# Kernel optimization log

Hardware: AMD Instinct MI355X
Metric: run time of the kernel (lower is better)

## Reference

```python
import jax, jax.numpy as jnp
import numpy as np
from jax import lax

B, C, H, W = 2, 96, 48, 48
BASE_C, HEADS, D_STATE, D_CONV, EXPAND = 32, 8, 16, 4, 2
D_INNER = EXPAND * C          # 192 (mamba expand=2)
DT_RANK = (C + 15) // 16      # 6  (ceil(d_model/16))
LN_EPS = 1e-5


def setup_inputs() -> dict:
    key = jax.random.key(0)
    ks = jax.random.split(key, 16)
    g = lambda i, shape, s=0.02: jax.random.normal(ks[i], shape, jnp.float32) * s
    return {
        "x": jax.random.normal(ks[0], (B, C, H, W), jnp.float32),
        "f_lu": jax.random.normal(ks[1], (B, BASE_C, 12, 12), jnp.float32),
        "norm_w": jnp.ones((C,), jnp.float32),
        "norm_b": jnp.zeros((C,), jnp.float32),
        "qproj_w": g(2, (C, BASE_C)), "qproj_b": jnp.zeros((C,), jnp.float32),
        "iq_w": g(3, (C, C)), "iq_b": jnp.zeros((C,), jnp.float32),
        "ik_w": g(4, (C, C)), "ik_b": jnp.zeros((C,), jnp.float32),
        "iv_w": g(5, (C, C)), "iv_b": jnp.zeros((C,), jnp.float32),
        "io_w": g(6, (C, C)), "io_b": jnp.zeros((C,), jnp.float32),
        "m_in_w": g(7, (2 * D_INNER, C)),
        "m_conv_w": g(8, (D_INNER, 1, D_CONV), 0.1),
        "m_conv_b": jnp.zeros((D_INNER,), jnp.float32),
        "m_xproj_w": g(9, (DT_RANK + 2 * D_STATE, D_INNER)),
        "m_dtproj_w": g(10, (D_INNER, DT_RANK), 0.1),
        "m_dtproj_b": jnp.full((D_INNER,), -4.6, jnp.float32),  # softplus ~= 0.01
        "m_Alog": jnp.log(jnp.broadcast_to(
            jnp.arange(1, D_STATE + 1, dtype=jnp.float32), (D_INNER, D_STATE))),
        "m_D": jnp.ones((D_INNER,), jnp.float32),
        "m_out_w": g(11, (C, D_INNER)),
        "out_w": g(12, (C, C)), "out_b": jnp.zeros((C,), jnp.float32),
    }


def _pw(t, w, b):  # 1x1 conv
    return jnp.einsum('bchw,oc->bohw', t, w) + b[:, None, None]


def reference(x, f_lu, norm_w, norm_b, qproj_w, qproj_b,
              iq_w, iq_b, ik_w, ik_b, iv_w, iv_b, io_w, io_b,
              m_in_w, m_conv_w, m_conv_b, m_xproj_w, m_dtproj_w, m_dtproj_b,
              m_Alog, m_D, m_out_w, out_w, out_b):
    b, c, h, w = x.shape
    l = h * w
    dk = c // HEADS
    res = x

    # LayerNorm over channel dim
    xt = x.transpose(0, 2, 3, 1)
    mu = xt.mean(-1, keepdims=True)
    var = ((xt - mu) ** 2).mean(-1, keepdims=True)
    xn = ((xt - mu) * lax.rsqrt(var + LN_EPS) * norm_w + norm_b).transpose(0, 3, 1, 2)

    # bilinear upsample (align_corners=False) + 1x1 proj
    f = jax.image.resize(f_lu, (b, BASE_C, h, w), method='bilinear')
    f = _pw(f, qproj_w, qproj_b)

    # IAI cross-attention: query from f, key/value from normalized x
    q = _pw(f, iq_w, iq_b).reshape(b, HEADS, dk, l)
    k = _pw(xn, ik_w, ik_b).reshape(b, HEADS, dk, l)
    v = _pw(xn, iv_w, iv_b).reshape(b, HEADS, dk, l)
    attn = jax.nn.softmax(jnp.einsum('bhdl,bhdm->bhlm', q, k) * (dk ** -0.5), axis=-1)
    o = jnp.einsum('bhlm,bhdm->bhdl', attn, v).reshape(b, c, h, w)
    o = _pw(o, io_w, io_b)

    # ---- Mamba block (canonical mamba_ssm forward) ----
    def mamba(u):  # u: [Bm, L, C]
        Bm, L, _ = u.shape
        xz = jnp.einsum('blc,dc->bld', u, m_in_w)           # [Bm,L,2*D_INNER]
        xi, zg = xz[..., :D_INNER], xz[..., D_INNER:]
        # causal depthwise conv1d (d_conv=4) + SiLU
        xc = xi.transpose(0, 2, 1)                           # [Bm,D_INNER,L]
        xc = jnp.pad(xc, ((0, 0), (0, 0), (D_CONV - 1, 0)))
        xc = lax.conv_general_dilated(
            xc, m_conv_w, (1,), 'VALID',
            dimension_numbers=('NCH', 'OIH', 'NCH'),
            feature_group_count=D_INNER)
        xc = jax.nn.silu(xc + m_conv_b[None, :, None]).transpose(0, 2, 1)  # [Bm,L,D_INNER]
        x_dbl = jnp.einsum('bld,ed->ble', xc, m_xproj_w)
        dt = x_dbl[..., :DT_RANK]
        Bs = x_dbl[..., DT_RANK:DT_RANK + D_STATE]           # [Bm,L,N]
        Cs = x_dbl[..., DT_RANK + D_STATE:]                  # [Bm,L,N]
        dt = jax.nn.softplus(jnp.einsum('blr,dr->bld', dt, m_dtproj_w) + m_dtproj_b)
        A = -jnp.exp(m_Alog)                                 # [D_INNER,N]
        dA = jnp.exp(dt[..., None] * A)                      # [Bm,L,D_INNER,N]
        dBx = dt[..., None] * Bs[:, :, None, :] * xc[..., None]
        def comb(e1, e2):
            a1, b1 = e1
            a2, b2 = e2
            return a1 * a2, a2 * b1 + b2
        _, hs = lax.associative_scan(comb, (dA, dBx), axis=1)  # [Bm,L,D_INNER,N]
        y = jnp.einsum('bldn,bln->bld', hs, Cs) + m_D * xc
        y = y * jax.nn.silu(zg)
        return jnp.einsum('bld,cd->blc', y, m_out_w)

    # DSFS: four directional scans, averaged
    dirs = jnp.stack([o, jnp.flip(o, 3), jnp.flip(o, 2), jnp.flip(o, (2, 3))], 0)
    z = dirs.reshape(4 * b, c, l).transpose(0, 2, 1)         # [4b,l,c]
    y = mamba(z)
    y = y.transpose(0, 2, 1).reshape(4, b, c, h, w)
    y = (y[0] + jnp.flip(y[1], 3) + jnp.flip(y[2], 2) + jnp.flip(y[3], (2, 3))) / 4.0

    return _pw(y, out_w, out_b) + res
```

## Files before the change

### kernel.cpp

```cpp
#include <hip/hip_runtime.h>

static constexpr int B_ = 2, C_ = 96, H_ = 48, W_ = 48, L_ = 2304;
static constexpr int HEADS_ = 8, DK_ = 12, BASEC_ = 32;
static constexpr int DI_ = 192, DS_ = 16, DCONV_ = 4, DTR_ = 6;
static constexpr int NCH_ = 16, CHL_ = 144;
static constexpr int KC_ = 288;
static constexpr int KT2_ = 48;

__device__ __forceinline__ float sigmoidf_(float x){ return 1.f/(1.f+__expf(-x)); }

__global__ __launch_bounds__(256) void ln_kernel(const float* __restrict__ x,
    const float* __restrict__ nw, const float* __restrict__ nb, float* __restrict__ xn)
{
  __shared__ float tile[96][65];
  __shared__ float muS[64], rsS[64];
  int p0 = blockIdx.x * 64;
  int b  = p0 / L_;
  int hw0 = p0 % L_;
  int tid = threadIdx.x;
  for (int idx = tid; idx < 96*64; idx += 256) {
    int c = idx >> 6, i = idx & 63;
    tile[c][i] = x[((size_t)b*96 + c)*L_ + hw0 + i];
  }
  __syncthreads();
  if (tid < 64) {
    float s = 0.f;
    #pragma unroll 8
    for (int c = 0; c < 96; ++c) s += tile[c][tid];
    float mu = s * (1.f/96.f);
    float v = 0.f;
    #pragma unroll 8
    for (int c = 0; c < 96; ++c) { float d = tile[c][tid]-mu; v += d*d; }
    v *= (1.f/96.f);
    muS[tid] = mu;
    rsS[tid] = rsqrtf(v + 1e-5f);
  }
  __syncthreads();
  for (int idx = tid; idx < 96*64; idx += 256) {
    int i = idx / 96, c = idx % 96;
    float val = (tile[c][i]-muS[i])*rsS[i]*nw[c] + nb[c];
    xn[((size_t)(p0 + i))*96 + c] = val;
  }
}

__global__ __launch_bounds__(256) void resize_kernel(const float* __restrict__ f, float* __restrict__ o)
{
  int t = blockIdx.x*256 + threadIdx.x;
  if (t >= B_*L_*BASEC_) return;
  int c = t & 31;
  int p = t >> 5;
  int w = p % 48, h = (p/48) % 48, b = p / (48*48);
  const float* a = f + ((size_t)b*32 + c)*144;
  float sh = (h+0.5f)*0.25f - 0.5f;
  float sw = (w+0.5f)*0.25f - 0.5f;
  int h0 = (int)floorf(sh); float fh = sh - (float)h0;
  int w0 = (int)floorf(sw); float fw = sw - (float)w0;
  int h0c = min(max(h0,0),11), h1c = min(max(h0+1,0),11);
  int w0c = min(max(w0,0),11), w1c = min(max(w0+1,0),11);
  float v00 = a[h0c*12+w0c], v01 = a[h0c*12+w1c];
  float v10 = a[h1c*12+w0c], v11 = a[h1c*12+w1c];
  o[t] = (1.f-fh)*((1.f-fw)*v00 + fw*v01) + fh*((1.f-fw)*v10 + fw*v11);
}

__global__ __launch_bounds__(256) void gemm_k(
    const float* __restrict__ A, int lda,
    const float* __restrict__ W,
    const float* __restrict__ bias,
    float* __restrict__ Co,
    int M, int N, int K,
    int act, int smode,
    const float* __restrict__ resid)
{
  __shared__ __align__(16) float As[16][68];
  __shared__ __align__(16) float Ws[16][68];
  int m0 = blockIdx.y*64, n0 = blockIdx.x*64;
  int tid = threadIdx.x;
  int tm = tid >> 4, tn = tid & 15;
  bool vec = ((K & 15) == 0) && ((lda & 3) == 0);
  float acc[4][4] = {};
  for (int k0 = 0; k0 < K; k0 += 16) {
    if (vec) {
      int row = tid >> 2, kq = (tid & 3) * 4;
      const float4 a4 = *(const float4*)&A[(size_t)(m0+row)*lda + k0 + kq];
      As[kq+0][row]=a4.x; As[kq+1][row]=a4.y; As[kq+2][row]=a4.z; As[kq+3][row]=a4.w;
      float4 w4 = make_float4(0.f,0.f,0.f,0.f);
      int nrow = n0 + row;
      if (nrow < N) w4 = *(const float4*)&W[(size_t)nrow*K + k0 + kq];
      Ws[kq+0][row]=w4.x; Ws[kq+1][row]=w4.y; Ws[kq+2][row]=w4.z; Ws[kq+3][row]=w4.w;
    } else {
      #pragma unroll
      for (int t = 0; t < 4; ++t) {
        int flat = tid + t*256;
        int i = flat >> 4, kk = flat & 15;
        int k = k0 + kk;
        float v = 0.f;
        if (k < K) v = A[(size_t)(m0+i)*lda + k];
        As[kk][i] = v;
      }
      #pragma unroll
      for (int t = 0; t < 4; ++t) {
        int flat = tid + t*256;
        int j = flat >> 4, kk = flat & 15;
        int k = k0 + kk, n = n0 + j;
        float v = 0.f;
        if (k < K && n < N) v = W[(size_t)n*K + k];
        Ws[kk][j] = v;
      }
    }
    __syncthreads();
    #pragma unroll
    for (int kk = 0; kk < 16; ++kk) {
      const float4 av = *(const float4*)&As[kk][tm*4];
      const float4 bv = *(const float4*)&Ws[kk][tn*4];
      float a[4] = {av.x, av.y, av.z, av.w};
      float b[4] = {bv.x, bv.y, bv.z, bv.w};
      #pragma unroll
      for (int i = 0; i < 4; ++i)
        #pragma unroll
        for (int j = 0; j < 4; ++j) acc[i][j] += a[i]*b[j];
    }
    __syncthreads();
  }
  #pragma unroll
  for (int i = 0; i < 4; ++i) {
    int m = m0 + tm*4 + i;
    #pragma unroll
    for (int j = 0; j < 4; ++j) {
      int n = n0 + tn*4 + j;
      if (n < N) {
        float v = acc[i][j];
        if (bias) v += bias[n];
        if (act == 1) v = fmaxf(v, 0.f) + log1pf(__expf(-fabsf(v)));
        if (smode == 0) {
          Co[(size_t)m*N + n] = v;
        } else {
          size_t o = ((size_t)(m / L_)*96 + n)*L_ + (m % L_);
          Co[o] = v + resid[o];
        }
      }
    }
  }
}

__global__ __launch_bounds__(128) void attn_part(const float* __restrict__ q,
    const float* __restrict__ k, const float* __restrict__ v, float* __restrict__ pbuf)
{
  __shared__ __align__(16) float ks[KT2_][12];
  __shared__ __align__(16) float vs[KT2_][12];
  int tid = threadIdx.x;
  int qt = blockIdx.x;
  int mc = blockIdx.y;
  int h  = blockIdx.z & 7, b = blockIdx.z >> 3;
  int q0 = qt*384 + tid*3;
  const float* qp = q + ((size_t)(b*L_ + q0))*96 + h*12;
  float qv[3][12];
  #pragma unroll
  for (int i = 0; i < 3; ++i)
    #pragma unroll
    for (int d = 0; d < 12; ++d)
      qv[i][d] = qp[(size_t)i*96 + d] * 0.28867513459481287f;
  float mx[3] = {-1e30f,-1e30f,-1e30f};
  float sm[3] = {};
  float acc[3][12] = {};
  const float* kbase = k + ((size_t)b*L_)*96 + h*12;
  const float* vbase = v + ((size_t)b*L_)*96 + h*12;
  int m0 = mc*KC_;
  for (int t0 = 0; t0 < KC_; t0 += KT2_) {
    __syncthreads();
    for (int it = tid; it < KT2_*3*2; it += 128) {
      int half = it / (KT2_*3);
      int rem  = it % (KT2_*3);
      int r = rem / 3, quad = rem % 3;
      const float* src = (half ? vbase : kbase) + (size_t)(m0 + t0 + r)*96 + quad*4;
      float4 val = *(const float4*)src;
      float* dst = half ? &vs[r][quad*4] : &ks[r][quad*4];
      *(float4*)dst = val;
    }
    __syncthreads();
    for (int mi = 0; mi < KT2_; ++mi) {
      float kr[12], vr[12];
      *(float4*)&kr[0] = *(const float4*)&ks[mi][0];
      *(float4*)&kr[4] = *(const float4*)&ks[mi][4];
      *(float4*)&kr[8] = *(const float4*)&ks[mi][8];
      float s[3] = {};
      #pragma unroll
      for (int i = 0; i < 3; ++i)
        #pragma unroll
        for (int d = 0; d < 12; ++d) s[i] += qv[i][d]*kr[d];
      *(float4*)&vr[0] = *(const float4*)&vs[mi][0];
      *(float4*)&vr[4] = *(const float4*)&vs[mi][4];
      *(float4*)&vr[8] = *(const float4*)&vs[mi][8];
      #pragma unroll
      for (int i = 0; i < 3; ++i) {
        if (s[i] > mx[i] + 12.f) {
          float corr = __expf(mx[i] - s[i]);
          mx[i] = s[i]; sm[i] *= corr;
          #pragma unroll
          for (int d = 0; d < 12; ++d) acc[i][d] *= corr;
        }
        float p = __expf(s[i] - mx[i]);
        sm[i] += p;
        #pragma unroll
        for (int d = 0; d < 12; ++d) acc[i][d] += p*vr[d];
      }
    }
  }
  int bh = b*8 + h;
  #pragma unroll
  for (int i = 0; i < 3; ++i) {
    float* o = pbuf + (((size_t)bh*8 + mc)*L_ + (q0 + i))*14;
    o[0] = mx[i]; o[1] = sm[i];
    #pragma unroll
    for (int d = 0; d < 12; ++d) o[2+d] = acc[i][d];
  }
}

__global__ __launch_bounds__(256) void attn_comb(const float* __restrict__ pbuf, float* __restrict__ aout)
{
  int t = blockIdx.x*256 + threadIdx.x;
  if (t >= 16*L_) return;
  int l = t % L_, bh = t / L_;
  float gm = -1e30f;
  #pragma unroll
  for (int mc = 0; mc < 8; ++mc) {
    const float* r = pbuf + (((size_t)bh*8 + mc)*L_ + l)*14;
    gm = fmaxf(gm, r[0]);
  }
  float tot = 0.f, acc[12] = {};
  #pragma unroll
  for (int mc = 0; mc < 8; ++mc) {
    const float* r = pbuf + (((size_t)bh*8 + mc)*L_ + l)*14;
    float w = __expf(r[0] - gm);
    tot += r[1]*w;
    #pragma unroll
    for (int d = 0; d < 12; ++d) acc[d] += r[2+d]*w;
  }
  int b = bh >> 3, h = bh & 7;
  float* o = aout + ((size_t)(b*L_ + l))*96 + h*12;
  float inv = 1.f/tot;
  #pragma unroll
  for (int d = 0; d < 12; ++d) o[d] = acc[d]*inv;
}

__global__ __launch_bounds__(256) void zgather(const float* __restrict__ ot, float* __restrict__ zin)
{
  int t = blockIdx.x*256 + threadIdx.x;
  if (t >= 8*L_*24) return;
  int cq = t % 24; int p = t / 24; int l = p % L_; int bbp = p / L_;
  int dir = bbp / B_, b = bbp % B_;
  int hh = l / 48, ww = l % 48;
  int wsrc = (dir & 1) ? 47 - ww : ww;
  int hsrc = (dir & 2) ? 47 - hh : hh;
  int lsrc = hsrc*48 + wsrc;
  float4 v = *(const float4*)&ot[((size_t)(b*L_) + lsrc)*96 + cq*4];
  *(float4*)&zin[(size_t)p*96 + cq*4] = v;
}

__global__ __launch_bounds__(256) void conv_kernel(const float* __restrict__ xz,
    const float* __restrict__ cw, const float* __restrict__ cb, float* __restrict__ xc)
{
  int t = blockIdx.x*256 + threadIdx.x;
  if (t >= 8*L_*48) return;
  int dq = t % 48; int p = t / 48; int l = p % L_;
  int d = dq*4;
  float s0 = cb[d], s1 = cb[d+1], s2 = cb[d+2], s3 = cb[d+3];
  #pragma unroll
  for (int kk = 0; kk < 4; ++kk) {
    int ls = l - 3 + kk;
    if (ls >= 0) {
      float4 xv = *(const float4*)&xz[(size_t)(p - 3 + kk)*384 + d];
      s0 += xv.x * cw[(d+0)*4 + kk];
      s1 += xv.y * cw[(d+1)*4 + kk];
      s2 += xv.z * cw[(d+2)*4 + kk];
      s3 += xv.w * cw[(d+3)*4 + kk];
    }
  }
  float4 r;
  r.x = s0 * sigmoidf_(s0);
  r.y = s1 * sigmoidf_(s1);
  r.z = s2 * sigmoidf_(s2);
  r.w = s3 * sigmoidf_(s3);
  *(float4*)&xc[(size_t)p*192 + d] = r;
}

__global__ __launch_bounds__(256) void scan_p1(const float* __restrict__ dtb,
    const float* __restrict__ xcb, const float* __restrict__ xdbl,
    const float* __restrict__ Alog, float* __restrict__ Parr, float* __restrict__ Harr)
{
  int seq = blockIdx.y >> 4;
  int ch  = blockIdx.y & 15;
  int d = blockIdx.x*16 + (threadIdx.x >> 4);
  int n = threadIdx.x & 15;
  float An = -__expf(Alog[d*16 + n]);
  float h = 0.f, P = 1.f;
  size_t base = (size_t)seq * L_ + (size_t)ch * CHL_;
  for (int l = 0; l < CHL_; ++l) {
    size_t p = base + l;
    float dtv = dtb[p*192 + d];
    float xcv = xcb[p*192 + d];
    float Bn  = xdbl[p*38 + 6 + n];
    float dA = __expf(dtv*An);
    h = dA*h + (dtv*xcv)*Bn;
    P *= dA;
  }
  size_t idx = (((size_t)seq*NCH_ + ch)*192 + d)*16 + n;
  Parr[idx] = P; Harr[idx] = h;
}

__global__ __launch_bounds__(256) void scan_p2(const float* __restrict__ Parr,
    const float* __restrict__ Harr, float* __restrict__ Hstart)
{
  int t = blockIdx.x*256 + threadIdx.x;
  if (t >= 8*192*16) return;
  int n = t & 15; int d = (t >> 4) % 192; int seq = t / (192*16);
  float Hc = 0.f;
  #pragma unroll
  for (int c = 0; c < NCH_; ++c) {
    size_t idx = (((size_t)seq*NCH_ + c)*192 + d)*16 + n;
    Hstart[idx] = Hc;
    Hc = Harr[idx] + Parr[idx]*Hc;
  }
}

__global__ __launch_bounds__(256) void scan_p3(const float* __restrict__ dtb,
    const float* __restrict__ xcb, const float* __restrict__ xdbl,
    const float* __restrict__ xz, const float* __restrict__ Alog,
    const float* __restrict__ Dp, const float* __restrict__ Hstart,
    float* __restrict__ ypre)
{
  int seq = blockIdx.y >> 4;
  int ch  = blockIdx.y & 15;
  int d = blockIdx.x*16 + (threadIdx.x >> 4);
  int n = threadIdx.x & 15;
  float An = -__expf(Alog[d*16 + n]);
  float Dd = Dp[d];
  size_t idx = (((size_t)seq*NCH_ + ch)*192 + d)*16 + n;
  float h = Hstart[idx];
  size_t base = (size_t)seq * L_ + (size_t)ch * CHL_;
  for (int l = 0; l < CHL_; ++l) {
    size_t p = base + l;
    float dtv = dtb[p*192 + d];
    float xcv = xcb[p*192 + d];
    float Bn  = xdbl[p*38 + 6 + n];
    float Cn  = xdbl[p*38 + 22 + n];
    float dA = __expf(dtv*An);
    h = dA*h + (dtv*xcv)*Bn;
    float c = h*Cn;
    c += __shfl_xor(c, 1);
    c += __shfl_xor(c, 2);
    c += __shfl_xor(c, 4);
    c += __shfl_xor(c, 8);
    if (n == 0) {
      float zg = xz[p*384 + 192 + d];
      float yv = c + Dd*xcv;
      yv *= zg * sigmoidf_(zg);
      ypre[p*192 + d] = yv;
    }
  }
}

__global__ __launch_bounds__(256) void ycomb(const float* __restrict__ ypre, float* __restrict__ ysum)
{
  int t = blockIdx.x*256 + threadIdx.x;
  if (t >= B_*L_*48) return;
  int dq = t % 48; int p = t / 48; int l = p % L_; int b = p / L_;
  int d = dq*4;
  int hh = l / 48, ww = l % 48;
  int l1 = hh*48 + (47 - ww);
  int l2 = (47 - hh)*48 + ww;
  int l3 = (47 - hh)*48 + (47 - ww);
  float4 v0 = *(const float4*)&ypre[(((size_t)(0*B_ + b)*L_ + l ))*192 + d];
  float4 v1 = *(const float4*)&ypre[(((size_t)(1*B_ + b)*L_ + l1))*192 + d];
  float4 v2 = *(const float4*)&ypre[(((size_t)(2*B_ + b)*L_ + l2))*192 + d];
  float4 v3 = *(const float4*)&ypre[(((size_t)(3*B_ + b)*L_ + l3))*192 + d];
  float4 r;
  r.x = (v0.x + v1.x + v2.x + v3.x) * 0.25f;
  r.y = (v0.y + v1.y + v2.y + v3.y) * 0.25f;
  r.z = (v0.z + v1.z + v2.z + v3.z) * 0.25f;
  r.w = (v0.w + v1.w + v2.w + v3.w) * 0.25f;
  *(float4*)&ysum[(size_t)p*192 + d] = r;
}

extern "C" void kernel_launch(void* const* d_in, const int* in_sizes, int n_in,
                              void* d_out, int out_size, void* d_ws, size_t ws_size,
                              hipStream_t stream)
{
  const float* x        = (const float*)d_in[0];
  const float* f_lu     = (const float*)d_in[1];
  const float* norm_w   = (const float*)d_in[2];
  const float* norm_b   = (const float*)d_in[3];
  const float* qproj_w  = (const float*)d_in[4];
  const float* qproj_b  = (const float*)d_in[5];
  const float* iq_w     = (const float*)d_in[6];
  const float* iq_b     = (const float*)d_in[7];
  const float* ik_w     = (const float*)d_in[8];
  const float* ik_b     = (const float*)d_in[9];
  const float* iv_w     = (const float*)d_in[10];
  const float* iv_b     = (const float*)d_in[11];
  const float* io_w     = (const float*)d_in[12];
  const float* io_b     = (const float*)d_in[13];
  const float* m_in_w   = (const float*)d_in[14];
  const float* m_conv_w = (const float*)d_in[15];
  const float* m_conv_b = (const float*)d_in[16];
  const float* m_xproj_w  = (const float*)d_in[17];
  const float* m_dtproj_w = (const float*)d_in[18];
  const float* m_dtproj_b = (const float*)d_in[19];
  const float* m_Alog   = (const float*)d_in[20];
  const float* m_D      = (const float*)d_in[21];
  const float* m_out_w  = (const float*)d_in[22];
  const float* out_w    = (const float*)d_in[23];
  const float* out_b    = (const float*)d_in[24];
  float* ws  = (float*)d_ws;
  float* out = (float*)d_out;

  float* XN   = ws + 0;
  float* F48  = ws + 442368;
  float* FQ   = ws + 589824;
  float* QT   = ws + 1032192;
  float* KT   = ws + 1474560;
  float* VT   = ws + 1916928;
  float* AOUT = ws + 589824;
  float* OT   = ws + 0;
  float* ZIN  = ws + 2359296;
  float* PART = ws + 4128768;
  float* XZ   = ws + 4128768;
  float* XC   = ws + 11206656;
  float* XDBL = ws + 14745600;
  float* DTB  = ws + 15446016;
  float* PARR = ws + 18984960;
  float* HARR = ws + 19771392;
  float* HST  = ws + 20557824;
  float* YPRE = ws + 0;
  float* YSUM = ws + 3538944;
  float* CVEC = ws + 4423680;

  ln_kernel<<<72, 256, 0, stream>>>(x, norm_w, norm_b, XN);
  resize_kernel<<<576, 256, 0, stream>>>(f_lu, F48);
  gemm_k<<<dim3(2,72),  256, 0, stream>>>(F48, 32, qproj_w, qproj_b, FQ, 4608, 96, 32, 0, 0, nullptr);
  gemm_k<<<dim3(2,72),  256, 0, stream>>>(FQ, 96, iq_w, iq_b, QT, 4608, 96, 96, 0, 0, nullptr);
  gemm_k<<<dim3(2,72),  256, 0, stream>>>(XN, 96, ik_w, ik_b, KT, 4608, 96, 96, 0, 0, nullptr);
  gemm_k<<<dim3(2,72),  256, 0, stream>>>(XN, 96, iv_w, iv_b, VT, 4608, 96, 96, 0, 0, nullptr);
  attn_part<<<dim3(6,8,16), 128, 0, stream>>>(QT, KT, VT, PART);
  attn_comb<<<144, 256, 0, stream>>>(PART, AOUT);
  gemm_k<<<dim3(2,72),  256, 0, stream>>>(AOUT, 96, io_w, io_b, OT, 4608, 96, 96, 0, 0, nullptr);
  zgather<<<1728, 256, 0, stream>>>(OT, ZIN);
  gemm_k<<<dim3(6,288), 256, 0, stream>>>(ZIN, 96, m_in_w, nullptr, XZ, 18432, 384, 96, 0, 0, nullptr);
  conv_kernel<<<3456, 256, 0, stream>>>(XZ, m_conv_w, m_conv_b, XC);
  gemm_k<<<dim3(1,288), 256, 0, stream>>>(XC, 192, m_xproj_w, nullptr, XDBL, 18432, 38, 192, 0, 0, nullptr);
  gemm_k<<<dim3(3,288), 256, 0, stream>>>(XDBL, 38, m_dtproj_w, m_dtproj_b, DTB, 18432, 192, 6, 1, 0, nullptr);
  scan_p1<<<dim3(12,128), 256, 0, stream>>>(DTB, XC, XDBL, m_Alog, PARR, HARR);
  scan_p2<<<96, 256, 0, stream>>>(PARR, HARR, HST);
  scan_p3<<<dim3(12,128), 256, 0, stream>>>(DTB, XC, XDBL, XZ, m_Alog, m_D, HST, YPRE);
  ycomb<<<864, 256, 0, stream>>>(YPRE, YSUM);
  gemm_k<<<dim3(2,72),  256, 0, stream>>>(YSUM, 192, m_out_w, nullptr, CVEC, 4608, 96, 192, 0, 0, nullptr);
  gemm_k<<<dim3(2,72),  256, 0, stream>>>(CVEC, 96, out_w, out_b, out, 4608, 96, 96, 0, 1, x);
}
```

Baseline: 568.3 us.

## Replace scalar split-K attention with fp16 MFMA flash attention

Adds a conversion kernel that writes Q (pre-scaled), K and transposed V to fp16, zero-padded to MFMA-friendly widths. A new single-wave attention kernel then computes QK^T and PV with 16x16x32 f16 MFMA instructions and an online softmax that only rescales when the running max grows past a threshold. This removes the fp32 scalar dot-product loops and the separate partial-combine pass with its partial buffer. The cost is fp16 precision on probabilities and inputs, plus wasted MFMA work on the zero padding (head dim 12 padded to 32 and 16).

Measured after the change: 496.2 us. 1.15x faster.

```diff
diff --git a/kernel.cpp b/kernel.cpp
--- a/kernel.cpp
+++ b/kernel.cpp
@@ -4,8 +4,9 @@
 static constexpr int HEADS_ = 8, DK_ = 12, BASEC_ = 32;
 static constexpr int DI_ = 192, DS_ = 16, DCONV_ = 4, DTR_ = 6;
 static constexpr int NCH_ = 16, CHL_ = 144;
-static constexpr int KC_ = 288;
-static constexpr int KT2_ = 48;
+
+using f16x8 = __attribute__((ext_vector_type(8))) _Float16;
+using f32x4 = __attribute__((ext_vector_type(4))) float;
 
 __device__ __forceinline__ float sigmoidf_(float x){ return 1.f/(1.f+__expf(-x)); }
 
@@ -142,104 +143,86 @@
   }
 }
 
-__global__ __launch_bounds__(128) void attn_part(const float* __restrict__ q,
-    const float* __restrict__ k, const float* __restrict__ v, float* __restrict__ pbuf)
-{
-  __shared__ __align__(16) float ks[KT2_][12];
-  __shared__ __align__(16) float vs[KT2_][12];
-  int tid = threadIdx.x;
+__global__ __launch_bounds__(64) void qkv2h(const float* __restrict__ QT,
+    const float* __restrict__ KT, const float* __restrict__ VT,
+    _Float16* __restrict__ Qh, _Float16* __restrict__ Kh, _Float16* __restrict__ VTh)
+{
+  int bh = blockIdx.x;
+  int l  = blockIdx.y*64 + threadIdx.x;
+  int b = bh >> 3, h = bh & 7;
+  size_t src = ((size_t)(b*L_ + l))*96 + h*12;
+  alignas(16) _Float16 qrow[32];
+  alignas(16) _Float16 krow[32];
+  #pragma unroll
+  for (int d = 0; d < 12; ++d) {
+    qrow[d] = (_Float16)(QT[src+d] * 0.28867513459481287f);
+    krow[d] = (_Float16)KT[src+d];
+  }
+  #pragma unroll
+  for (int d = 12; d < 32; ++d) { qrow[d] = (_Float16)0.f; krow[d] = (_Float16)0.f; }
+  _Float16* qdst = Qh + ((size_t)(bh*L_ + l))*32;
+  _Float16* kdst = Kh + ((size_t)(bh*L_ + l))*32;
+  #pragma unroll
+  for (int t = 0; t < 4; ++t) {
+    *(uint4*)(qdst + t*8) = *(const uint4*)&qrow[t*8];
+    *(uint4*)(kdst + t*8) = *(const uint4*)&krow[t*8];
+  }
+  #pragma unroll
+  for (int d = 0; d < 12; ++d)
+    VTh[((size_t)(bh*16 + d))*L_ + l] = (_Float16)VT[src+d];
+  #pragma unroll
+  for (int d = 12; d < 16; ++d)
+    VTh[((size_t)(bh*16 + d))*L_ + l] = (_Float16)0.f;
+}
+
+__global__ __launch_bounds__(64) void attn_mfma(
+    const _Float16* __restrict__ Qh, const _Float16* __restrict__ Kh,
+    const _Float16* __restrict__ VTh, float* __restrict__ aout)
+{
+  int lane = threadIdx.x;
   int qt = blockIdx.x;
-  int mc = blockIdx.y;
-  int h  = blockIdx.z & 7, b = blockIdx.z >> 3;
-  int q0 = qt*384 + tid*3;
-  const float* qp = q + ((size_t)(b*L_ + q0))*96 + h*12;
-  float qv[3][12];
-  #pragma unroll
-  for (int i = 0; i < 3; ++i)
-    #pragma unroll
-    for (int d = 0; d < 12; ++d)
-      qv[i][d] = qp[(size_t)i*96 + d] * 0.28867513459481287f;
-  float mx[3] = {-1e30f,-1e30f,-1e30f};
-  float sm[3] = {};
-  float acc[3][12] = {};
-  const float* kbase = k + ((size_t)b*L_)*96 + h*12;
-  const float* vbase = v + ((size_t)b*L_)*96 + h*12;
-  int m0 = mc*KC_;
-  for (int t0 = 0; t0 < KC_; t0 += KT2_) {
-    __syncthreads();
-    for (int it = tid; it < KT2_*3*2; it += 128) {
-      int half = it / (KT2_*3);
-      int rem  = it % (KT2_*3);
-      int r = rem / 3, quad = rem % 3;
-      const float* src = (half ? vbase : kbase) + (size_t)(m0 + t0 + r)*96 + quad*4;
-      float4 val = *(const float4*)src;
-      float* dst = half ? &vs[r][quad*4] : &ks[r][quad*4];
-      *(float4*)dst = val;
-    }
-    __syncthreads();
-    for (int mi = 0; mi < KT2_; ++mi) {
-      float kr[12], vr[12];
-      *(float4*)&kr[0] = *(const float4*)&ks[mi][0];
-      *(float4*)&kr[4] = *(const float4*)&ks[mi][4];
-      *(float4*)&kr[8] = *(const float4*)&ks[mi][8];
-      float s[3] = {};
-      #pragma unroll
-      for (int i = 0; i < 3; ++i)
-        #pragma unroll
-        for (int d = 0; d < 12; ++d) s[i] += qv[i][d]*kr[d];
-      *(float4*)&vr[0] = *(const float4*)&vs[mi][0];
-      *(float4*)&vr[4] = *(const float4*)&vs[mi][4];
-      *(float4*)&vr[8] = *(const float4*)&vs[mi][8];
-      #pragma unroll
-      for (int i = 0; i < 3; ++i) {
-        if (s[i] > mx[i] + 12.f) {
-          float corr = __expf(mx[i] - s[i]);
-          mx[i] = s[i]; sm[i] *= corr;
-          #pragma unroll
-          for (int d = 0; d < 12; ++d) acc[i][d] *= corr;
-        }
-        float p = __expf(s[i] - mx[i]);
-        sm[i] += p;
-        #pragma unroll
-        for (int d = 0; d < 12; ++d) acc[i][d] += p*vr[d];
-      }
-    }
-  }
-  int bh = b*8 + h;
-  #pragma unroll
-  for (int i = 0; i < 3; ++i) {
-    float* o = pbuf + (((size_t)bh*8 + mc)*L_ + (q0 + i))*14;
-    o[0] = mx[i]; o[1] = sm[i];
-    #pragma unroll
-    for (int d = 0; d < 12; ++d) o[2+d] = acc[i][d];
-  }
-}
-
-__global__ __launch_bounds__(256) void attn_comb(const float* __restrict__ pbuf, float* __restrict__ aout)
-{
-  int t = blockIdx.x*256 + threadIdx.x;
-  if (t >= 16*L_) return;
-  int l = t % L_, bh = t / L_;
-  float gm = -1e30f;
-  #pragma unroll
-  for (int mc = 0; mc < 8; ++mc) {
-    const float* r = pbuf + (((size_t)bh*8 + mc)*L_ + l)*14;
-    gm = fmaxf(gm, r[0]);
-  }
-  float tot = 0.f, acc[12] = {};
-  #pragma unroll
-  for (int mc = 0; mc < 8; ++mc) {
-    const float* r = pbuf + (((size_t)bh*8 + mc)*L_ + l)*14;
-    float w = __expf(r[0] - gm);
-    tot += r[1]*w;
-    #pragma unroll
-    for (int d = 0; d < 12; ++d) acc[d] += r[2+d]*w;
-  }
-  int b = bh >> 3, h = bh & 7;
-  float* o = aout + ((size_t)(b*L_ + l))*96 + h*12;
-  float inv = 1.f/tot;
-  #pragma unroll
-  for (int d = 0; d < 12; ++d) o[d] = acc[d]*inv;
+  int bh = blockIdx.y;
+  int a = lane & 15, g = lane >> 4;
+  const f16x8 qf = *(const f16x8*)(Qh + ((size_t)(bh*L_ + qt*16 + a))*32 + g*8);
+  f32x4 o = {0.f,0.f,0.f,0.f};
+  float m = -1e30f, s = 0.f;
+  const _Float16* kb = Kh + (size_t)bh*L_*32;
+  const _Float16* vb = VTh + ((size_t)(bh*16 + a))*L_;
+  int krow0 = 8*(a>>2) + (a&3);
+  for (int kt = 0; kt < L_; kt += 32) {
+    const f16x8 kf0 = *(const f16x8*)(kb + (size_t)(kt + krow0    )*32 + g*8);
+    const f16x8 kf1 = *(const f16x8*)(kb + (size_t)(kt + krow0 + 4)*32 + g*8);
+    f32x4 z = {0.f,0.f,0.f,0.f};
+    f32x4 st0 = __builtin_amdgcn_mfma_f32_16x16x32_f16(kf0, qf, z, 0, 0, 0);
+    f32x4 st1 = __builtin_amdgcn_mfma_f32_16x16x32_f16(kf1, qf, z, 0, 0, 0);
+    float tm = fmaxf(fmaxf(fmaxf(st0[0],st0[1]),fmaxf(st0[2],st0[3])),
+                     fmaxf(fmaxf(st1[0],st1[1]),fmaxf(st1[2],st1[3])));
+    tm = fmaxf(tm, __shfl_xor(tm, 16));
+    tm = fmaxf(tm, __shfl_xor(tm, 32));
+    if (!__all(tm <= m + 10.f)) {
+      float nm = fmaxf(m, tm);
+      float corr = __expf(m - nm);
+      s *= corr;
+      o[0]*=corr; o[1]*=corr; o[2]*=corr; o[3]*=corr;
+      m = nm;
+    }
+    float p0=__expf(st0[0]-m), p1=__expf(st0[1]-m), p2=__expf(st0[2]-m), p3=__expf(st0[3]-m);
+    float p4=__expf(st1[0]-m), p5=__expf(st1[1]-m), p6=__expf(st1[2]-m), p7=__expf(st1[3]-m);
+    s += (p0+p1)+(p2+p3)+(p4+p5)+(p6+p7);
+    f16x8 pf;
+    pf[0]=(_Float16)p0; pf[1]=(_Float16)p1; pf[2]=(_Float16)p2; pf[3]=(_Float16)p3;
+    pf[4]=(_Float16)p4; pf[5]=(_Float16)p5; pf[6]=(_Float16)p6; pf[7]=(_Float16)p7;
+    const f16x8 vf = *(const f16x8*)(vb + kt + g*8);
+    o = __builtin_amdgcn_mfma_f32_16x16x32_f16(vf, pf, o, 0, 0, 0);
+  }
+  s += __shfl_xor(s, 16);
+  s += __shfl_xor(s, 32);
+  float inv = 1.f / s;
+  if (g < 3) {
+    int b = bh >> 3, h = bh & 7;
+    float4 r; r.x = o[0]*inv; r.y = o[1]*inv; r.z = o[2]*inv; r.w = o[3]*inv;
+    *(float4*)&aout[((size_t)(b*L_ + qt*16 + a))*96 + h*12 + g*4] = r;
+  }
 }
 
 __global__ __launch_bounds__(256) void zgather(const float* __restrict__ ot, float* __restrict__ zin)
@@ -422,7 +405,9 @@
   float* AOUT = ws + 589824;
   float* OT   = ws + 0;
   float* ZIN  = ws + 2359296;
-  float* PART = ws + 4128768;
+  _Float16* QH  = (_Float16*)(ws + 4128768);
+  _Float16* KH  = (_Float16*)(ws + 5308416);
+  _Float16* VTH = (_Float16*)(ws + 6488064);
   float* XZ   = ws + 4128768;
   float* XC   = ws + 11206656;
   float* XDBL = ws + 14745600;
@@ -440,8 +425,8 @@
   gemm_k<<<dim3(2,72),  256, 0, stream>>>(FQ, 96, iq_w, iq_b, QT, 4608, 96, 96, 0, 0, nullptr);
   gemm_k<<<dim3(2,72),  256, 0, stream>>>(XN, 96, ik_w, ik_b, KT, 4608, 96, 96, 0, 0, nullptr);
   gemm_k<<<dim3(2,72),  256, 0, stream>>>(XN, 96, iv_w, iv_b, VT, 4608, 96, 96, 0, 0, nullptr);
-  attn_part<<<dim3(6,8,16), 128, 0, stream>>>(QT, KT, VT, PART);
-  attn_comb<<<144, 256, 0, stream>>>(PART, AOUT);
+  qkv2h<<<dim3(16,36), 64, 0, stream>>>(QT, KT, VT, QH, KH, VTH);
+  attn_mfma<<<dim3(144,16), 64, 0, stream>>>(QH, KH, VTH, AOUT);
   gemm_k<<<dim3(2,72),  256, 0, stream>>>(AOUT, 96, io_w, io_b, OT, 4608, 96, 96, 0, 0, nullptr);
   zgather<<<1728, 256, 0, stream>>>(OT, ZIN);
   gemm_k<<<dim3(6,288), 256, 0, stream>>>(ZIN, 96, m_in_w, nullptr, XZ, 18432, 384, 96, 0, 0, nullptr);
```
